# Optimization experiments

Hardware: AMD Instinct MI355X
Metric: run time of the kernel (lower is better)

## Reference

```python
import jax, jax.numpy as jnp
import numpy as np

B, S, HID, OP, NVAR = 4096, 1024, 30, 30, 4
# norm table passed as [[0,1],...,[0,1]] -> norm[0]=(0,1), norm[4]=(0,1)
N00, N01, N40, N41 = 0.0, 1.0, 0.0, 1.0


def setup_inputs() -> dict:
    key = jax.random.key(0)
    k = jax.random.split(key, 12)
    f32 = jnp.float32
    return {
        "x": jax.random.normal(k[0], (B, S, 4), f32),
        "var": jax.random.normal(k[1], (B, NVAR), f32),
        "amps": jax.random.uniform(k[2], (B, 2), f32, 0.5, 1.5),
        "s0": jnp.zeros((B, OP), f32),
        "W_dnn1": jax.random.normal(k[3], (1, OP + NVAR), f32) * 0.1,
        "b_dnn1": jnp.zeros((1,), f32),
        "W_x2h": jax.random.normal(k[4], (HID, 7), f32) * 0.2,
        "W_h2h": jax.random.normal(k[5], (HID, HID), f32) * 0.1,
        "W_dnn2": jax.random.normal(k[6], (1, HID), f32) * 0.1 + 0.2,
        "b_dnn2": jnp.zeros((1,), f32),
        "W_m1": jax.random.normal(k[7], (64, NVAR + 1), f32) * 0.1,
        "b_m1": jnp.zeros((64,), f32),
        "W_m2": jax.random.normal(k[8], (32, 64), f32) * 0.1,
        "b_m2": jnp.zeros((32,), f32),
        "W_m3": jax.random.normal(k[9], (1, 32), f32) * 0.1,
        "b_m3": jnp.zeros((1,), f32),
        "n_init": 16,
    }


def reference(x, var, amps, s0, W_dnn1, b_dnn1, W_x2h, W_h2h, W_dnn2, b_dnn2,
              W_m1, b_m1, W_m2, b_m2, W_m3, b_m3, n_init):
    dt = x.dtype
    # stop-operator thresholds: linspace(5/OP, 5, OP), shape (1, OP)
    r = jnp.linspace(5.0 / OP, 5.0, OP, dtype=dt).reshape(1, OP)
    x2 = jnp.concatenate([x[:, :, 0:1], x[:, :, 2:4]], axis=2)  # (B,S,3)
    dB = x[:, :, 1:2]  # (B,S,1)

    def hyst(s):  # dnn1 over concat(stop-operator state, var)
        return jnp.concatenate([s, var], axis=1) @ W_dnn1.T + b_dnn1  # (B,1)

    # --- t = 0 (special init of the eddy hidden state) ---
    s1 = jnp.clip((dB[:, 0] + s0) / r, -1.0, 1.0) * r  # (B,OP)
    H_hyst0 = hyst(s1)
    H_eddy_init = x[:, 0, 0:1] - H_hyst0  # (B,1)
    h2 = jnp.ones((x.shape[0], HID), dt) / jnp.sum(W_dnn2, axis=1) * H_eddy_init
    h2 = jax.nn.sigmoid(jnp.concatenate([x2[:, 0], var], axis=1) @ W_x2h.T + h2 @ W_h2h.T)
    H0 = H_hyst0 + h2 @ W_dnn2.T + b_dnn2  # (B,1)

    # --- t = 1..S-1 via scan ---
    def step(carry, xs):
        s1, h2 = carry
        dB_t, x2_t = xs  # (B,1), (B,3)
        s1 = jnp.clip((dB_t + s1) / r, -1.0, 1.0) * r
        H_hyst = hyst(s1)
        h2 = jax.nn.sigmoid(jnp.concatenate([x2_t, var], axis=1) @ W_x2h.T + h2 @ W_h2h.T)
        return (s1, h2), H_hyst + h2 @ W_dnn2.T + b_dnn2

    xs = (jnp.swapaxes(dB[:, 1:], 0, 1), jnp.swapaxes(x2[:, 1:], 0, 1))
    _, Hs = jax.lax.scan(step, (s1, h2), xs)  # (S-1,B,1)
    output = jnp.concatenate([H0[:, None, :], jnp.swapaxes(Hs, 0, 1)], axis=1)  # (B,S,1)

    H = output[:, n_init:, :]
    B_amp = x[:, n_init:, 0:1] * amps[:, 0:1][:, None, :]
    H_amp = H * amps[:, 1:2][:, None, :]
    # trapezoid rule along time axis with non-uniform x spacing
    dxb = B_amp[:, 1:] - B_amp[:, :-1]
    P_prelim = jnp.sum(dxb * (H_amp[:, 1:] + H_amp[:, :-1]) * 0.5, axis=1)  # (B,1)
    P_prelim = P_prelim * 10.0 ** (var[:, 0:1] * N01 + N00)
    Pcv = (jnp.log10(jnp.clip(P_prelim, 1e-12)) - N40) / N41

    # loss MLP (eval mode: dropout = identity)
    mlp_in = jnp.concatenate([var, Pcv], axis=1)  # (B,5)
    h = jax.nn.relu(mlp_in @ W_m1.T + b_m1)
    h = jax.nn.relu(h @ W_m2.T + b_m2)
    s = h @ W_m3.T + b_m3
    return H, Pcv + s
```

## Files before the change

kernel.cpp:

```cpp
#include <hip/hip_runtime.h>

#define B_TOT 4096
#define S_LEN 1024
#define HID 30
#define SKIP 16
#define HLEN (S_LEN - SKIP)
#define WARM 32

typedef float f32x16 __attribute__((ext_vector_type(16)));
typedef short bf16x8 __attribute__((ext_vector_type(8)));
typedef int   i32x4  __attribute__((ext_vector_type(4)));
typedef unsigned int u32x2 __attribute__((ext_vector_type(2)));

template <int CTRL>
__device__ __forceinline__ float dppmov(float v) {
  return __int_as_float(__builtin_amdgcn_update_dpp(
      0, __float_as_int(v), CTRL, 0xF, 0xF, true));
}
template <int CTRL>
__device__ __forceinline__ float dpp_add(float v) { return v + dppmov<CTRL>(v); }
__device__ __forceinline__ float red16(float v) {
  v = dpp_add<0xB1>(v); v = dpp_add<0x4E>(v);
  v = dpp_add<0x141>(v); v = dpp_add<0x140>(v);
  return v;
}
__device__ __forceinline__ float sigmoid_fast(float z) {
  float e = __builtin_amdgcn_exp2f(z * -1.442695041f);
  return __builtin_amdgcn_rcpf(1.0f + e);
}
__device__ __forceinline__ int cvt_pk_bf16(float a, float b) {
  int r; asm("v_cvt_pk_bf16_f32 %0, %1, %2" : "=v"(r) : "v"(a), "v"(b)); return r;
}
__device__ __forceinline__ void split8(const float* v, int* hw, int* lw) {
#pragma unroll
  for (int p = 0; p < 4; ++p) {
    int h = cvt_pk_bf16(v[2*p], v[2*p+1]);
    float f0 = __int_as_float(h << 16);
    float f1 = __int_as_float(h & 0xffff0000);
    lw[p] = cvt_pk_bf16(v[2*p] - f0, v[2*p+1] - f1);
    hw[p] = h;
  }
}
__device__ __forceinline__ bf16x8 frag4(const int* w) {
  return __builtin_bit_cast(bf16x8, (i32x4){w[0], w[1], w[2], w[3]});
}

__device__ __forceinline__ float redh(float v) {
#if __has_builtin(__builtin_amdgcn_permlane32_swap)
  unsigned iv = __float_as_uint(v);
  u32x2 qq = __builtin_amdgcn_permlane32_swap(iv, iv, false, false);
  return __uint_as_float(qq[0]) + __uint_as_float(qq[1]);
#else
  int l = (int)(threadIdx.x & 63);
  v += __int_as_float(__builtin_amdgcn_ds_bpermute(((l ^ 32) << 2),
                                                   __float_as_int(v)));
  return v;
#endif
}

__global__ __launch_bounds__(256, 1) void mminet_scan(
    const float* __restrict__ x,   const float* __restrict__ var,
    const float* __restrict__ s0,
    const float* __restrict__ W1,  const float* __restrict__ b1,
    const float* __restrict__ Wx,  const float* __restrict__ Wh,
    const float* __restrict__ W2,  const float* __restrict__ b2,
    float* __restrict__ Hout, float* __restrict__ Pws)
{
  __shared__ float Pred[4][32];

  const int tid   = threadIdx.x;
  const int l     = tid & 63;
  const int cl    = tid >> 6;
  const int half  = blockIdx.x & 1;
  const int g     = blockIdx.x >> 1;
  const int hi    = l >> 5;
  const int cb    = l & 31;
  const int b     = g * 32 + cb;

  const int ob = (half == 0)
      ? (cl == 0 ? 16  : cl == 1 ? 160 : cl == 2 ? 288 : 408)
      : (cl == 0 ? 520 : cl == 1 ? 648 : cl == 2 ? 776 : 900);
  const int oe = (half == 0)
      ? (cl == 0 ? 160 : cl == 1 ? 288 : cl == 2 ? 408 : 520)
      : (cl == 0 ? 648 : cl == 1 ? 776 : cl == 2 ? 900 : 1024);
  const bool first = (half == 0) && (cl == 0);
  const int ps = first ? SKIP : ((ob - WARM) & ~31);

  const float v0 = var[b*4+0], v1 = var[b*4+1], v2 = var[b*4+2], v3 = var[b*4+3];

  float wx0[16], wx1[16], wx2[16], cva[16], w1a[16], w2a[16], rc[16], s1[16];
#pragma unroll
  for (int r = 0; r < 16; ++r) {
    const int row = (r & 3) + 8 * (r >> 2) + 4 * hi;
    if (row < HID) {
      wx0[r] = Wx[row*7+0]; wx1[r] = Wx[row*7+1]; wx2[r] = Wx[row*7+2];
      cva[r] = Wx[row*7+3]*v0 + Wx[row*7+4]*v1 + Wx[row*7+5]*v2 + Wx[row*7+6]*v3;
      w1a[r] = W1[row]; w2a[r] = W2[row];
      rc[r]  = 5.0f * (float)(row + 1) / 30.0f;
      s1[r]  = s0[b*HID + row];
    } else {
      wx0[r]=wx1[r]=wx2[r]=cva[r]=w1a[r]=w2a[r]=s1[r]=0.f; rc[r]=1.0f;
    }
  }

  float a1v[8], a2v[8];
#pragma unroll
  for (int j = 0; j < 8; ++j) {
    const int u1 = (j & 3) + 8 * (j >> 2) + 4 * hi;
    const int u2 = 16 + u1;
    a1v[j] = (cb < HID) ? Wh[cb*HID + u1] : 0.f;
    a2v[j] = (cb < HID && u2 < HID) ? Wh[cb*HID + u2] : 0.f;
  }
  int t0[4], t1[4], t2[4], t3[4];
  split8(a1v, t0, t1); split8(a2v, t2, t3);
  const bf16x8 A1h = frag4(t0), A1l = frag4(t1);
  const bf16x8 A2h = frag4(t2), A2l = frag4(t3);

  const float hcst = W1[30]*v0 + W1[31]*v1 + W1[32]*v2 + W1[33]*v3 + b1[0];
  const float hc2  = hcst + b2[0];

  float sw = 0.f;
#pragma unroll
  for (int r = 0; r < 16; ++r) sw += w2a[r];
  const float sumW2 = redh(sw);

  const float4* xb = (const float4*)(x + (size_t)b * S_LEN * 4);

  bf16x8 B1h, B1l, B2h, B2l;
  auto packB = [&](const float* hv) {
    int bh[4], bl[4];
    split8(hv, bh, bl);      B1h = frag4(bh); B1l = frag4(bl);
    split8(hv + 8, bh, bl);  B2h = frag4(bh); B2l = frag4(bl);
  };

  auto dostep = [&](const float4 xq) -> float {
#pragma unroll
    for (int r = 0; r < 16; ++r)
      s1[r] = __builtin_amdgcn_fmed3f(s1[r] + xq.y, -rc[r], rc[r]);
    f32x16 acc;
#pragma unroll
    for (int r = 0; r < 16; ++r)
      acc[r] = cva[r] + wx0[r]*xq.x + wx1[r]*xq.z + wx2[r]*xq.w;
    acc = __builtin_amdgcn_mfma_f32_32x32x16_bf16(A1h, B1h, acc, 0, 0, 0);
    acc = __builtin_amdgcn_mfma_f32_32x32x16_bf16(A2h, B2h, acc, 0, 0, 0);
    acc = __builtin_amdgcn_mfma_f32_32x32x16_bf16(A1l, B1h, acc, 0, 0, 0);
    acc = __builtin_amdgcn_mfma_f32_32x32x16_bf16(A2l, B2h, acc, 0, 0, 0);
    acc = __builtin_amdgcn_mfma_f32_32x32x16_bf16(A1h, B1l, acc, 0, 0, 0);
    acc = __builtin_amdgcn_mfma_f32_32x32x16_bf16(A2h, B2l, acc, 0, 0, 0);
    float hv[16];
#pragma unroll
    for (int r = 0; r < 16; ++r) hv[r] = sigmoid_fast(acc[r]);
    packB(hv);
    float hp = 0.f;
#pragma unroll
    for (int r = 0; r < 16; ++r)
      hp = fmaf(w1a[r], s1[r], fmaf(w2a[r], hv[r], hp));
    return redh(hp);
  };

  if (first) {
    float4 xv = xb[0];
#pragma unroll
    for (int r = 0; r < 16; ++r)
      s1[r] = __builtin_amdgcn_fmed3f(s1[r] + xv.y, -rc[r], rc[r]);
    float hh = 0.f;
#pragma unroll
    for (int r = 0; r < 16; ++r) hh = fmaf(w1a[r], s1[r], hh);
    const float Hh0  = redh(hh) + hcst;
    const float hpre = (xv.x - Hh0) / sumW2;
    float hv[16];
#pragma unroll
    for (int r = 0; r < 16; ++r) {
      const int row = (r & 3) + 8 * (r >> 2) + 4 * hi;
      float rs = 0.f;
      if (row < HID)
        for (int u = 0; u < HID; ++u) rs += Wh[row*HID + u];
      float z = cva[r] + wx0[r]*xv.x + wx1[r]*xv.z + wx2[r]*xv.w + rs*hpre;
      hv[r] = sigmoid_fast(z);
    }
    packB(hv);
    for (int t = 1; t < SKIP; ++t) (void)dostep(xb[t]);
  } else {
    const float* xf = x + (size_t)b * S_LEN * 4;
    float dc[32], dn[32];
#pragma unroll
    for (int u = 0; u < 32; ++u) dc[u] = xf[u*4 + 1];
    for (int t = 0; t < ps; t += 32) {
      const bool more = (t + 32 < ps);
      if (more) {
#pragma unroll
        for (int u = 0; u < 32; ++u) dn[u] = xf[(t + 32 + u)*4 + 1];
      }
#pragma unroll
      for (int u = 0; u < 32; ++u) {
#pragma unroll
        for (int r = 0; r < 16; ++r)
          s1[r] = __builtin_amdgcn_fmed3f(s1[r] + dc[u], -rc[r], rc[r]);
      }
      if (more) {
#pragma unroll
        for (int u = 0; u < 32; ++u) dc[u] = dn[u];
      }
    }
    float hv[16];
#pragma unroll
    for (int r = 0; r < 16; ++r) hv[r] = 0.5f;
    packB(hv);
  }

  float P = 0.f, Hprev = 0.f, Bprev = 0.f;
  float4 xc0 = xb[ps+0], xc1 = xb[ps+1], xc2 = xb[ps+2], xc3 = xb[ps+3];

  for (int t = ps; t < oe; t += 4) {
    const int tn = (t + 4 < oe) ? (t + 4) : t;
    float4 xn0 = xb[tn+0], xn1 = xb[tn+1], xn2 = xb[tn+2], xn3 = xb[tn+3];

    float hq0, hq1, hq2, hq3;
    {
      float Ht = dostep(xc0) + hc2;
      if (t + 0 > SKIP && t + 0 >= ob) P += (xc0.x - Bprev) * (Ht + Hprev);
      Hprev = Ht; Bprev = xc0.x; hq0 = Ht;
    }
    {
      float Ht = dostep(xc1) + hc2;
      if (t + 1 > SKIP && t + 1 >= ob) P += (xc1.x - Bprev) * (Ht + Hprev);
      Hprev = Ht; Bprev = xc1.x; hq1 = Ht;
    }
    {
      float Ht = dostep(xc2) + hc2;
      if (t + 2 > SKIP && t + 2 >= ob) P += (xc2.x - Bprev) * (Ht + Hprev);
      Hprev = Ht; Bprev = xc2.x; hq2 = Ht;
    }
    {
      float Ht = dostep(xc3) + hc2;
      if (t + 3 > SKIP && t + 3 >= ob) P += (xc3.x - Bprev) * (Ht + Hprev);
      Hprev = Ht; Bprev = xc3.x; hq3 = Ht;
    }
    if (t >= ob && l < 32) {
      *(float4*)(Hout + (size_t)b * HLEN + (t - SKIP)) =
          make_float4(hq0, hq1, hq2, hq3);
    }
    xc0 = xn0; xc1 = xn1; xc2 = xn2; xc3 = xn3;
  }

  if (l < 32) Pred[cl][cb] = P;
  __syncthreads();
  if (tid < 32) {
    const int bb = g * 32 + tid;
    Pws[bb * 2 + half] =
        Pred[0][tid] + Pred[1][tid] + Pred[2][tid] + Pred[3][tid];
  }
}

__global__ __launch_bounds__(256) void mminet_mlp(
    const float* __restrict__ var, const float* __restrict__ amps,
    const float* __restrict__ Wm1, const float* __restrict__ bm1,
    const float* __restrict__ Wm2, const float* __restrict__ bm2,
    const float* __restrict__ Wm3, const float* __restrict__ bm3,
    const float* __restrict__ Pws, float* __restrict__ out2)
{
  __shared__ float mlpbuf[16][64];
  const int tid = threadIdx.x;
  const int li  = tid & 15;
  const int g   = tid >> 4;
  const int be  = blockIdx.x * 16 + g;

  const float Ptot = Pws[be*2 + 0] + Pws[be*2 + 1];
  const float e0 = var[be*4+0], e1 = var[be*4+1], e2 = var[be*4+2], e3 = var[be*4+3];
  const float am0 = amps[be*2+0], am1 = amps[be*2+1];

  float Pp = Ptot * 0.5f * am0 * am1;
  Pp *= __builtin_amdgcn_exp2f(e0 * 3.321928095f);
  Pp = fmaxf(Pp, 1e-12f);
  const float Pcv = __builtin_amdgcn_logf(Pp) * 0.30102999566f;

  float* hs = &mlpbuf[g][0];
#pragma unroll
  for (int qq = 0; qq < 4; ++qq) {
    const int n = li + 16 * qq;
    const float* wr = Wm1 + n * 5;
    float h1v = bm1[n] + wr[0]*e0 + wr[1]*e1 + wr[2]*e2 + wr[3]*e3 + wr[4]*Pcv;
    hs[n] = fmaxf(h1v, 0.f);
  }
  const int m0 = li, m1 = li + 16;
  const float4* h1v4 = (const float4*)hs;
  const float4* w2a4 = (const float4*)(Wm2 + m0 * 64);
  const float4* w2b4 = (const float4*)(Wm2 + m1 * 64);
  float zz0 = bm2[m0], zz1 = bm2[m1];
#pragma unroll
  for (int qq = 0; qq < 16; ++qq) {
    float4 hh = h1v4[qq];
    float4 wa = w2a4[qq], wb = w2b4[qq];
    zz0 += wa.x*hh.x + wa.y*hh.y + wa.z*hh.z + wa.w*hh.w;
    zz1 += wb.x*hh.x + wb.y*hh.y + wb.z*hh.z + wb.w*hh.w;
  }
  float sp = Wm3[m0] * fmaxf(zz0, 0.f) + Wm3[m1] * fmaxf(zz1, 0.f);
  sp = red16(sp);
  if (li == 0) out2[be] = Pcv + sp + bm3[0];
}

extern "C" void kernel_launch(void* const* d_in, const int* in_sizes, int n_in,
                              void* d_out, int out_size, void* d_ws, size_t ws_size,
                              hipStream_t stream)
{
  const float* x    = (const float*)d_in[0];
  const float* var  = (const float*)d_in[1];
  const float* amps = (const float*)d_in[2];
  const float* s0   = (const float*)d_in[3];
  const float* W1   = (const float*)d_in[4];
  const float* b1   = (const float*)d_in[5];
  const float* Wx   = (const float*)d_in[6];
  const float* Wh   = (const float*)d_in[7];
  const float* W2   = (const float*)d_in[8];
  const float* b2   = (const float*)d_in[9];
  const float* Wm1  = (const float*)d_in[10];
  const float* bm1  = (const float*)d_in[11];
  const float* Wm2  = (const float*)d_in[12];
  const float* bm2  = (const float*)d_in[13];
  const float* Wm3  = (const float*)d_in[14];
  const float* bm3  = (const float*)d_in[15];

  float* Hout = (float*)d_out;
  float* out2 = (float*)d_out + (size_t)B_TOT * HLEN;
  float* Pws  = (float*)d_ws;

  mminet_scan<<<(B_TOT / 32) * 2, 256, 0, stream>>>(
      x, var, s0, W1, b1, Wx, Wh, W2, b2, Hout, Pws);
  mminet_mlp<<<B_TOT / 16, 256, 0, stream>>>(
      var, amps, Wm1, bm1, Wm2, bm2, Wm3, bm3, Pws, out2);
}
```

Measured before the change: 294.0 us.

## Fold two input projections into MFMA padding slots and rebalance time segments

Moves the Wx columns for x.x and x.z into the unused K slots (rows 30,31) of the recurrent weight matrix. The next step's inputs are packed into the B fragment, so the MFMA computes those projections and the per-step VALU FMAs and registers drop. It also rebalances the per-wave time-segment boundaries and shrinks the warm-up prefetch buffer from 32 to 8. The cost is bf16 hi/lo splitting of raw x inputs, which slightly changes precision, and more complex boundary handling at segment edges.

```diff
diff --git a/kernel.cpp b/kernel.cpp
--- a/kernel.cpp
+++ b/kernel.cpp
@@ -78,28 +78,28 @@
   const int b     = g * 32 + cb;
 
   const int ob = (half == 0)
-      ? (cl == 0 ? 16  : cl == 1 ? 160 : cl == 2 ? 288 : 408)
-      : (cl == 0 ? 520 : cl == 1 ? 648 : cl == 2 ? 776 : 900);
+      ? (cl == 0 ? 16  : cl == 1 ? 188 : cl == 2 ? 340 : 484)
+      : (cl == 0 ? 608 : cl == 1 ? 728 : cl == 2 ? 832 : 932);
   const int oe = (half == 0)
-      ? (cl == 0 ? 160 : cl == 1 ? 288 : cl == 2 ? 408 : 520)
-      : (cl == 0 ? 648 : cl == 1 ? 776 : cl == 2 ? 900 : 1024);
+      ? (cl == 0 ? 188 : cl == 1 ? 340 : cl == 2 ? 484 : 608)
+      : (cl == 0 ? 728 : cl == 1 ? 832 : cl == 2 ? 932 : 1024);
   const bool first = (half == 0) && (cl == 0);
   const int ps = first ? SKIP : ((ob - WARM) & ~31);
 
   const float v0 = var[b*4+0], v1 = var[b*4+1], v2 = var[b*4+2], v3 = var[b*4+3];
 
-  float wx0[16], wx1[16], wx2[16], cva[16], w1a[16], w2a[16], rc[16], s1[16];
+  float wx2[16], cva[16], w1a[16], w2a[16], rc[16], s1[16];
 #pragma unroll
   for (int r = 0; r < 16; ++r) {
     const int row = (r & 3) + 8 * (r >> 2) + 4 * hi;
     if (row < HID) {
-      wx0[r] = Wx[row*7+0]; wx1[r] = Wx[row*7+1]; wx2[r] = Wx[row*7+2];
+      wx2[r] = Wx[row*7+2];
       cva[r] = Wx[row*7+3]*v0 + Wx[row*7+4]*v1 + Wx[row*7+5]*v2 + Wx[row*7+6]*v3;
       w1a[r] = W1[row]; w2a[r] = W2[row];
       rc[r]  = 5.0f * (float)(row + 1) / 30.0f;
       s1[r]  = s0[b*HID + row];
     } else {
-      wx0[r]=wx1[r]=wx2[r]=cva[r]=w1a[r]=w2a[r]=s1[r]=0.f; rc[r]=1.0f;
+      wx2[r]=cva[r]=w1a[r]=w2a[r]=s1[r]=0.f; rc[r]=1.0f;
     }
   }
 
@@ -110,6 +110,10 @@
     const int u2 = 16 + u1;
     a1v[j] = (cb < HID) ? Wh[cb*HID + u1] : 0.f;
     a2v[j] = (cb < HID && u2 < HID) ? Wh[cb*HID + u2] : 0.f;
+  }
+  if (hi) {
+    a2v[6] = (cb < HID) ? Wx[cb*7+0] : 0.f;
+    a2v[7] = (cb < HID) ? Wx[cb*7+1] : 0.f;
   }
   int t0[4], t1[4], t2[4], t3[4];
   split8(a1v, t0, t1); split8(a2v, t2, t3);
@@ -133,14 +137,14 @@
     split8(hv + 8, bh, bl);  B2h = frag4(bh); B2l = frag4(bl);
   };
 
-  auto dostep = [&](const float4 xq) -> float {
+  auto dostep = [&](const float4 xq, const float4 xn) -> float {
 #pragma unroll
     for (int r = 0; r < 16; ++r)
       s1[r] = __builtin_amdgcn_fmed3f(s1[r] + xq.y, -rc[r], rc[r]);
     f32x16 acc;
 #pragma unroll
     for (int r = 0; r < 16; ++r)
-      acc[r] = cva[r] + wx0[r]*xq.x + wx1[r]*xq.z + wx2[r]*xq.w;
+      acc[r] = fmaf(wx2[r], xq.w, cva[r]);
     acc = __builtin_amdgcn_mfma_f32_32x32x16_bf16(A1h, B1h, acc, 0, 0, 0);
     acc = __builtin_amdgcn_mfma_f32_32x32x16_bf16(A2h, B2h, acc, 0, 0, 0);
     acc = __builtin_amdgcn_mfma_f32_32x32x16_bf16(A1l, B1h, acc, 0, 0, 0);
@@ -150,16 +154,18 @@
     float hv[16];
 #pragma unroll
     for (int r = 0; r < 16; ++r) hv[r] = sigmoid_fast(acc[r]);
-    packB(hv);
     float hp = 0.f;
 #pragma unroll
     for (int r = 0; r < 16; ++r)
       hp = fmaf(w1a[r], s1[r], fmaf(w2a[r], hv[r], hp));
+    if (hi) { hv[14] = xn.x; hv[15] = xn.z; }
+    packB(hv);
     return redh(hp);
   };
 
   if (first) {
     float4 xv = xb[0];
+    float4 x1 = xb[1];
 #pragma unroll
     for (int r = 0; r < 16; ++r)
       s1[r] = __builtin_amdgcn_fmed3f(s1[r] + xv.y, -rc[r], rc[r]);
@@ -172,39 +178,43 @@
 #pragma unroll
     for (int r = 0; r < 16; ++r) {
       const int row = (r & 3) + 8 * (r >> 2) + 4 * hi;
-      float rs = 0.f;
-      if (row < HID)
+      float rs = 0.f, w0 = 0.f, w1x = 0.f;
+      if (row < HID) {
         for (int u = 0; u < HID; ++u) rs += Wh[row*HID + u];
-      float z = cva[r] + wx0[r]*xv.x + wx1[r]*xv.z + wx2[r]*xv.w + rs*hpre;
+        w0 = Wx[row*7+0]; w1x = Wx[row*7+1];
+      }
+      float z = cva[r] + w0*xv.x + w1x*xv.z + wx2[r]*xv.w + rs*hpre;
       hv[r] = sigmoid_fast(z);
     }
+    if (hi) { hv[14] = x1.x; hv[15] = x1.z; }
     packB(hv);
-    for (int t = 1; t < SKIP; ++t) (void)dostep(xb[t]);
+    for (int t = 1; t < SKIP; ++t) (void)dostep(xb[t], xb[t + 1]);
   } else {
     const float* xf = x + (size_t)b * S_LEN * 4;
-    float dc[32], dn[32];
-#pragma unroll
-    for (int u = 0; u < 32; ++u) dc[u] = xf[u*4 + 1];
-    for (int t = 0; t < ps; t += 32) {
-      const bool more = (t + 32 < ps);
+    float dc[8], dn[8];
+#pragma unroll
+    for (int u = 0; u < 8; ++u) dc[u] = xf[u*4 + 1];
+    for (int t = 0; t < ps; t += 8) {
+      const bool more = (t + 8 < ps);
       if (more) {
 #pragma unroll
-        for (int u = 0; u < 32; ++u) dn[u] = xf[(t + 32 + u)*4 + 1];
+        for (int u = 0; u < 8; ++u) dn[u] = xf[(t + 8 + u)*4 + 1];
       }
 #pragma unroll
-      for (int u = 0; u < 32; ++u) {
+      for (int u = 0; u < 8; ++u) {
 #pragma unroll
         for (int r = 0; r < 16; ++r)
           s1[r] = __builtin_amdgcn_fmed3f(s1[r] + dc[u], -rc[r], rc[r]);
       }
       if (more) {
 #pragma unroll
-        for (int u = 0; u < 32; ++u) dc[u] = dn[u];
+        for (int u = 0; u < 8; ++u) dc[u] = dn[u];
       }
     }
     float hv[16];
 #pragma unroll
     for (int r = 0; r < 16; ++r) hv[r] = 0.5f;
+    if (hi) { float4 x0 = xb[ps]; hv[14] = x0.x; hv[15] = x0.z; }
     packB(hv);
   }
 
@@ -217,22 +227,22 @@
 
     float hq0, hq1, hq2, hq3;
     {
-      float Ht = dostep(xc0) + hc2;
+      float Ht = dostep(xc0, xc1) + hc2;
       if (t + 0 > SKIP && t + 0 >= ob) P += (xc0.x - Bprev) * (Ht + Hprev);
       Hprev = Ht; Bprev = xc0.x; hq0 = Ht;
     }
     {
-      float Ht = dostep(xc1) + hc2;
+      float Ht = dostep(xc1, xc2) + hc2;
       if (t + 1 > SKIP && t + 1 >= ob) P += (xc1.x - Bprev) * (Ht + Hprev);
       Hprev = Ht; Bprev = xc1.x; hq1 = Ht;
     }
     {
-      float Ht = dostep(xc2) + hc2;
+      float Ht = dostep(xc2, xc3) + hc2;
       if (t + 2 > SKIP && t + 2 >= ob) P += (xc2.x - Bprev) * (Ht + Hprev);
       Hprev = Ht; Bprev = xc2.x; hq2 = Ht;
     }
     {
-      float Ht = dostep(xc3) + hc2;
+      float Ht = dostep(xc3, xn0) + hc2;
       if (t + 3 > SKIP && t + 3 >= ob) P += (xc3.x - Bprev) * (Ht + Hprev);
       Hprev = Ht; Bprev = xc3.x; hq3 = Ht;
     }
```

Result: no change. 289.0 us (-1.7%).
